# Performance work log

Hardware: AMD Instinct MI355X
Metric: run time of the kernel (lower is better)

The kernel has to match this reference:

```python
import jax, jax.numpy as jnp
import numpy as np

B, L, D = 2, 2048, 1024
H = 16
DH = D // H
DFF = 4096
THETA = 10000.0
EPS = 1e-5


def setup_inputs() -> dict:
    key = jax.random.key(0)
    ks = jax.random.split(key, 6)
    s_qkv = (2.0 / (D + 3 * D)) ** 0.5
    s_o = (2.0 / (D + D)) ** 0.5
    s_ff = (2.0 / (D + DFF)) ** 0.5
    return {
        'x': jax.random.normal(ks[0], (B, L, D), jnp.float32),
        'w_qkv': jax.random.normal(ks[1], (3 * D, D), jnp.float32) * s_qkv,
        'w_o': jax.random.normal(ks[2], (D, D), jnp.float32) * s_o,
        'w1': jax.random.normal(ks[3], (DFF, D), jnp.float32) * s_ff,
        'w2': jax.random.normal(ks[4], (D, DFF), jnp.float32) * s_ff,
        'w3': jax.random.normal(ks[5], (DFF, D), jnp.float32) * s_ff,
        'g1': jnp.ones((D,), jnp.float32),
        'g2': jnp.ones((D,), jnp.float32),
    }


def _rmsnorm(x, g):
    xf = x.astype(jnp.float32)
    inv = jax.lax.rsqrt(jnp.mean(xf * xf, axis=-1, keepdims=True) + EPS)
    return (xf * inv * g).astype(x.dtype)


def _rotate_pair(t):
    # interleaved pairs: (x0,x1,x2,x3,...) -> (-x1,x0,-x3,x2,...)
    t2 = t.reshape(t.shape[:-1] + (t.shape[-1] // 2, 2))
    r = jnp.stack((-t2[..., 1], t2[..., 0]), axis=-1)
    return r.reshape(t.shape)


def reference(x, w_qkv, w_o, w1, w2, w3, g1, g2):
    Bb, Ll, Dd = x.shape
    # --- attention sublayer ---
    y = _rmsnorm(x, g1)
    qkv = y @ w_qkv.T                       # (B, L, 3D)
    q, k, v = jnp.split(qkv, 3, axis=-1)
    def to_heads(t):
        return t.reshape(Bb, Ll, H, DH).transpose(0, 2, 1, 3)  # (B,H,L,Dh)
    q, k, v = to_heads(q), to_heads(k), to_heads(v)
    # RoPE (interleaved), positions = 0..L-1
    inv_freq = 1.0 / (THETA ** (jnp.arange(0, DH, 2, dtype=jnp.float32) / DH))
    ang = jnp.arange(Ll, dtype=jnp.float32)[:, None] * inv_freq  # (L, Dh/2)
    ang = jnp.repeat(ang, 2, axis=-1)                            # (L, Dh)
    cos, sin = jnp.cos(ang), jnp.sin(ang)
    q = q * cos + _rotate_pair(q) * sin
    k = k * cos + _rotate_pair(k) * sin
    att = jnp.einsum('bhqd,bhkd->bhqk', q, k) * (1.0 / np.sqrt(DH))
    causal = jnp.tril(jnp.ones((Ll, Ll), dtype=bool))
    att = jnp.where(causal, att, -jnp.inf)
    att = jax.nn.softmax(att, axis=-1)
    yh = jnp.einsum('bhqk,bhkd->bhqd', att, v)
    y = yh.transpose(0, 2, 1, 3).reshape(Bb, Ll, Dd)
    x = x + y @ w_o.T
    # --- SwiGLU FFN sublayer ---
    y = _rmsnorm(x, g2)
    h = jax.nn.silu(y @ w1.T) * (y @ w3.T)
    return x + h @ w2.T
```

## Files before the change

kernel.cpp:

```cpp
#include <hip/hip_runtime.h>


typedef __attribute__((ext_vector_type(8))) short short8;
typedef __attribute__((ext_vector_type(4))) float f32x4;

#define DEV __device__ __forceinline__

DEV unsigned short f2b(float f) {
  unsigned int u = __builtin_bit_cast(unsigned int, f);
  unsigned int r = u + 0x7fffu + ((u >> 16) & 1u);
  return (unsigned short)(r >> 16);
}
DEV f32x4 MFMA(short8 a, short8 b, f32x4 c) {
  return __builtin_amdgcn_mfma_f32_16x16x32_bf16(a, b, c, 0, 0, 0);
}
DEV void gload16(const void* g, void* lds) {
  __builtin_amdgcn_global_load_lds((const __attribute__((address_space(1))) void*)g,
                                   (__attribute__((address_space(3))) void*)lds, 16, 0, 0);
}

__global__ __launch_bounds__(256) void cvt_k(const float* __restrict__ src,
                                             unsigned short* __restrict__ dst, int n) {
  int i = (blockIdx.x * 256 + threadIdx.x) * 4;
  if (i + 3 < n) {
    float4 v = *(const float4*)(src + i);
    ushort4 o;
    o.x = f2b(v.x); o.y = f2b(v.y); o.z = f2b(v.z); o.w = f2b(v.w);
    *(ushort4*)(dst + i) = o;
  } else {
    for (int c = 0; c < 4 && i + c < n; ++c) dst[i + c] = f2b(src[i + c]);
  }
}

__global__ __launch_bounds__(256) void rope_k(float2* __restrict__ tab) {
  const int i = blockIdx.x * 256 + threadIdx.x;
  const int lt = i >> 5, pr = i & 31;
  const float invf = __expf((float)pr * -0.28782313662425572f);
  const float ang = (float)lt * invf;
  float sn, cs;
  sincosf(ang, &sn, &cs);
  tab[i] = make_float2(cs, sn);
}

__global__ __launch_bounds__(256) void rms_k(const float* __restrict__ x,
                                             const float* __restrict__ g,
                                             unsigned short* __restrict__ out) {
  const int row = blockIdx.x;
  const int t = threadIdx.x;
  const float4 v = *(const float4*)(x + (size_t)row * 1024 + t * 4);
  float ss = v.x * v.x + v.y * v.y + v.z * v.z + v.w * v.w;
#pragma unroll
  for (int m = 32; m >= 1; m >>= 1) ss += __shfl_xor(ss, m, 64);
  __shared__ float red[4];
  if ((t & 63) == 0) red[t >> 6] = ss;
  __syncthreads();
  float tot = red[0] + red[1] + red[2] + red[3];
  float inv = rsqrtf(tot * (1.0f / 1024.0f) + 1e-5f);
  ushort4 o;
  o.x = f2b(v.x * inv * g[t * 4 + 0]);
  o.y = f2b(v.y * inv * g[t * 4 + 1]);
  o.z = f2b(v.z * inv * g[t * 4 + 2]);
  o.w = f2b(v.w * inv * g[t * 4 + 3]);
  *(ushort4*)(out + (size_t)row * 1024 + t * 4) = o;
}

template <int MODE>
__global__ __launch_bounds__(256, 3) void gemm_bt(
    const unsigned short* __restrict__ A, const unsigned short* __restrict__ B0,
    int M, int N, int K,
    float* __restrict__ outF, const float* __restrict__ resid,
    unsigned short* __restrict__ q, unsigned short* __restrict__ k2,
    unsigned short* __restrict__ v,
    const float2* __restrict__ rtab) {
  __shared__ __align__(16) unsigned short As[128 * 32];
  __shared__ __align__(16) unsigned short Bs[128 * 32];
  const int t = threadIdx.x;
  const int wv = t >> 6, ln = t & 63;
  const int l15 = ln & 15, grp = ln >> 4;
  const int wr = wv >> 1, wc = wv & 1;
  const int m0 = blockIdx.y * 128;
  const int n0 = blockIdx.x * 128;

  f32x4 acc[4][4];
#pragma unroll
  for (int mm = 0; mm < 4; ++mm)
#pragma unroll
    for (int nn = 0; nn < 4; ++nn) acc[mm][nn] = (f32x4){0.f, 0.f, 0.f, 0.f};

  for (int k0 = 0; k0 < K; k0 += 32) {
#pragma unroll
    for (int i = 0; i < 2; ++i) {
      const size_t rA = (size_t)(m0 + i * 64 + (t >> 2));
      gload16((const char*)A + (rA * K + k0) * 2 + (t & 3) * 16,
              (char*)As + i * 4096 + wv * 1024);
      const size_t rB = (size_t)(n0 + i * 64 + (t >> 2));
      gload16((const char*)B0 + (rB * K + k0) * 2 + (t & 3) * 16,
              (char*)Bs + i * 4096 + wv * 1024);
    }
    __syncthreads();
    short8 af[4], bf0[4];
#pragma unroll
    for (int mm = 0; mm < 4; ++mm)
      af[mm] = *(const short8*)&As[(wr * 64 + mm * 16 + l15) * 32 + grp * 8];
#pragma unroll
    for (int nn = 0; nn < 4; ++nn)
      bf0[nn] = *(const short8*)&Bs[(wc * 64 + nn * 16 + l15) * 32 + grp * 8];
#pragma unroll
    for (int mm = 0; mm < 4; ++mm)
#pragma unroll
      for (int nn = 0; nn < 4; ++nn) acc[mm][nn] = MFMA(af[mm], bf0[nn], acc[mm][nn]);
    __syncthreads();
  }

#pragma unroll
  for (int mm = 0; mm < 4; ++mm)
#pragma unroll
    for (int nn = 0; nn < 4; ++nn)
#pragma unroll
      for (int j = 0; j < 4; ++j) {
        const int r = m0 + wr * 64 + mm * 16 + grp * 4 + j;
        const int c = n0 + wc * 64 + nn * 16 + l15;
        float val = acc[mm][nn][j];
        if constexpr (MODE == 0) {
          const int mat = c >> 10;
          const int rem = c & 1023;
          const int hh = rem >> 6;
          const int dh = rem & 63;
          const int bt = r >> 11;
          const int lt = r & 2047;
          float outv = val;
          if (mat < 2) {
            const float partner = __shfl_xor(val, 1, 64);
            const float2 cs = rtab[lt * 32 + (dh >> 1)];
            outv = (dh & 1) ? (val * cs.x + partner * cs.y) : (val * cs.x - partner * cs.y);
          }
          unsigned short* dst = (mat == 0) ? q : ((mat == 1) ? k2 : v);
          dst[((size_t)(bt * 16 + hh) * 2048 + lt) * 64 + dh] = f2b(outv);
        } else {
          const size_t idx = (size_t)r * N + c;
          outF[idx] = resid[idx] + val;
        }
      }
}

__global__ __launch_bounds__(512, 2) void ffn_k(
    const unsigned short* __restrict__ A, const unsigned short* __restrict__ B0,
    const unsigned short* __restrict__ B1, unsigned short* __restrict__ outH) {
  __shared__ __align__(16) char Asm[2][32768];
  __shared__ __align__(16) char Bsm[2][32768];
  const int t = threadIdx.x;
  const int wid = t >> 6, lane = t & 63;
  const int l15 = lane & 15, grp = lane >> 4;
  const int wr = wid >> 2, wc = wid & 3;
  const int m0 = blockIdx.y * 256;
  const int n0 = blockIdx.x * 256;

  const char* srcA[4];
  const char* srcB[4];
#pragma unroll
  for (int s = 0; s < 4; ++s) {
    const int lb = s * 8192 + t * 16;
    const int r = lb >> 7;
    const int sw = (((lb >> 4) & 7) * 16) ^ ((r & 7) << 4);
    srcA[s] = (const char*)A + (size_t)(m0 + r) * 2048 + sw;
    const int R = n0 + r;
    const unsigned short* bsrc = ((R >> 4) & 1) ? B1 : B0;
    const int br = ((R >> 5) << 4) + (R & 15);
    srcB[s] = (const char*)bsrc + (size_t)br * 2048 + sw;
  }

  f32x4 acc[8][4];
#pragma unroll
  for (int m = 0; m < 8; ++m)
#pragma unroll
    for (int n = 0; n < 4; ++n) acc[m][n] = (f32x4){0.f, 0.f, 0.f, 0.f};

  gload16(srcA[0], Asm[0] + 0 * 8192 + wid * 1024);
  gload16(srcA[1], Asm[0] + 1 * 8192 + wid * 1024);
  gload16(srcB[0], Bsm[0] + 0 * 8192 + wid * 1024);
  gload16(srcB[1], Bsm[0] + 1 * 8192 + wid * 1024);
  gload16(srcA[2], Asm[0] + 2 * 8192 + wid * 1024);
  gload16(srcA[3], Asm[0] + 3 * 8192 + wid * 1024);
  gload16(srcB[2], Bsm[0] + 2 * 8192 + wid * 1024);
  gload16(srcB[3], Bsm[0] + 3 * 8192 + wid * 1024);

  const int rA0 = wr * 64 + l15;
  const int rB0 = wc * 32 + l15;

#pragma unroll 1
  for (int kt = 0; kt < 16; ++kt) {
    const int cb = kt & 1;
    const size_t koff = (size_t)((kt + 1 < 16) ? (kt + 1) : kt) * 128;
    const char* Ab = Asm[cb];
    const char* Bb = Bsm[cb];
    char* An = Asm[cb ^ 1];
    char* Bn = Bsm[cb ^ 1];

    short8 a0[2][4], a1[2][4], b0[2][2], b1[2][2];

    gload16(srcA[0] + koff, An + 0 * 8192 + wid * 1024);
    gload16(srcA[1] + koff, An + 1 * 8192 + wid * 1024);
    asm volatile("s_waitcnt vmcnt(6)" ::: "memory");
    __builtin_amdgcn_s_barrier();
#pragma unroll
    for (int ks = 0; ks < 2; ++ks)
#pragma unroll
      for (int m = 0; m < 4; ++m) {
        const int r = rA0 + m * 16;
        a0[ks][m] = *(const short8*)(Ab + r * 128 + ((ks * 64 + grp * 16) ^ ((r & 7) << 4)));
      }
#pragma unroll
    for (int ks = 0; ks < 2; ++ks)
#pragma unroll
      for (int n = 0; n < 2; ++n) {
        const int r = rB0 + n * 16;
        b0[ks][n] = *(const short8*)(Bb + r * 128 + ((ks * 64 + grp * 16) ^ ((r & 7) << 4)));
      }
    __builtin_amdgcn_sched_barrier(0);
    __builtin_amdgcn_s_setprio(1);
#pragma unroll
    for (int ks = 0; ks < 2; ++ks)
#pragma unroll
      for (int m = 0; m < 4; ++m)
#pragma unroll
        for (int n = 0; n < 2; ++n) acc[m][n] = MFMA(a0[ks][m], b0[ks][n], acc[m][n]);
    __builtin_amdgcn_s_setprio(0);

    gload16(srcB[0] + koff, Bn + 0 * 8192 + wid * 1024);
    gload16(srcB[1] + koff, Bn + 1 * 8192 + wid * 1024);
    asm volatile("s_waitcnt vmcnt(4)" ::: "memory");
    __builtin_amdgcn_s_barrier();
#pragma unroll
    for (int ks = 0; ks < 2; ++ks)
#pragma unroll
      for (int n = 0; n < 2; ++n) {
        const int r = 128 + rB0 + n * 16;
        b1[ks][n] = *(const short8*)(Bb + r * 128 + ((ks * 64 + grp * 16) ^ ((r & 7) << 4)));
      }
    __builtin_amdgcn_sched_barrier(0);
    __builtin_amdgcn_s_setprio(1);
#pragma unroll
    for (int ks = 0; ks < 2; ++ks)
#pragma unroll
      for (int m = 0; m < 4; ++m)
#pragma unroll
        for (int n = 0; n < 2; ++n) acc[m][2 + n] = MFMA(a0[ks][m], b1[ks][n], acc[m][2 + n]);
    __builtin_amdgcn_s_setprio(0);

    gload16(srcA[2] + koff, An + 2 * 8192 + wid * 1024);
    gload16(srcA[3] + koff, An + 3 * 8192 + wid * 1024);
    __builtin_amdgcn_s_barrier();
#pragma unroll
    for (int ks = 0; ks < 2; ++ks)
#pragma unroll
      for (int m = 0; m < 4; ++m) {
        const int r = 128 + rA0 + m * 16;
        a1[ks][m] = *(const short8*)(Ab + r * 128 + ((ks * 64 + grp * 16) ^ ((r & 7) << 4)));
      }
    __builtin_amdgcn_sched_barrier(0);
    __builtin_amdgcn_s_setprio(1);
#pragma unroll
    for (int ks = 0; ks < 2; ++ks)
#pragma unroll
      for (int m = 0; m < 4; ++m)
#pragma unroll
        for (int n = 0; n < 2; ++n) acc[4 + m][2 + n] = MFMA(a1[ks][m], b1[ks][n], acc[4 + m][2 + n]);
    __builtin_amdgcn_s_setprio(0);

    gload16(srcB[2] + koff, Bn + 2 * 8192 + wid * 1024);
    gload16(srcB[3] + koff, Bn + 3 * 8192 + wid * 1024);
    __builtin_amdgcn_s_barrier();
    __builtin_amdgcn_s_setprio(1);
#pragma unroll
    for (int ks = 0; ks < 2; ++ks)
#pragma unroll
      for (int m = 0; m < 4; ++m)
#pragma unroll
        for (int n = 0; n < 2; ++n) acc[4 + m][n] = MFMA(a1[ks][m], b0[ks][n], acc[4 + m][n]);
    __builtin_amdgcn_s_setprio(0);
  }

#pragma unroll
  for (int mh = 0; mh < 2; ++mh)
#pragma unroll
    for (int m = 0; m < 4; ++m)
#pragma unroll
      for (int nh = 0; nh < 2; ++nh)
#pragma unroll
        for (int j = 0; j < 4; ++j) {
          const int row = m0 + mh * 128 + wr * 64 + m * 16 + grp * 4 + j;
          const int ch = (n0 >> 1) + nh * 64 + wc * 16 + l15;
          const float a1v = acc[mh * 4 + m][nh * 2 + 0][j];
          const float a3v = acc[mh * 4 + m][nh * 2 + 1][j];
          const float hval = a1v / (1.0f + __expf(-a1v)) * a3v;
          outH[(size_t)row * 4096 + ch] = f2b(hval);
        }
}

__global__ __launch_bounds__(256) void vtr_k(const unsigned short* __restrict__ v,
                                             unsigned short* __restrict__ vt) {
  __shared__ __align__(16) unsigned short tile[64][72];
  const int bh = blockIdx.y;
  const int lt0 = blockIdx.x * 64;
  const int t = threadIdx.x;
  const int r = t >> 2;
  const int c0 = (t & 3) * 16;
  const unsigned short* src = v + ((size_t)bh * 2048 + lt0 + r) * 64 + c0;
  *(short8*)&tile[r][c0] = *(const short8*)src;
  *(short8*)&tile[r][c0 + 8] = *(const short8*)(src + 8);
  __syncthreads();
  unsigned short outv[16];
#pragma unroll
  for (int i = 0; i < 16; ++i) outv[i] = tile[c0 + i][r];
  unsigned short* dst = vt + ((size_t)bh * 64 + r) * 2048 + lt0 + c0;
  *(short8*)dst = *(short8*)&outv[0];
  *(short8*)(dst + 8) = *(short8*)&outv[8];
}

__global__ __launch_bounds__(256) void attn_k(const unsigned short* __restrict__ qb,
                                              const unsigned short* __restrict__ kb,
                                              const unsigned short* __restrict__ vt,
                                              unsigned short* __restrict__ yh) {
  const int pair = blockIdx.x;
  const int bh = blockIdx.y;
  const int t = threadIdx.x;
  const int w = t >> 6, lane = t & 63;
  const int l15 = lane & 15, grp = lane >> 4;

  __shared__ __align__(16) char Ks[2][8192];
  __shared__ __align__(16) char Vs[2][8192];
  __shared__ __align__(16) char Ps[8192];
  char* Pw = Ps + w * 2048;

  const char* kg = (const char*)kb + (size_t)bh * 262144;
  const char* vg = (const char*)vt + (size_t)bh * 262144;

  const int lb0 = t * 16, lb1 = 4096 + t * 16;
  const int r0 = lb0 >> 7, r1 = lb1 >> 7;
  const int sl0 = (lb0 & 0x70) ^ ((r0 & 7) << 4);
  const int sl1 = (lb1 & 0x70) ^ ((r1 & 7) << 4);
  const char* srcK0 = kg + r0 * 128 + sl0;
  const char* srcK1 = kg + r1 * 128 + sl1;
  const char* srcV0 = vg + (size_t)r0 * 4096 + sl0;
  const char* srcV1 = vg + (size_t)r1 * 4096 + sl1;

  const int bq = bh >> 4, hh = bh & 15;

#pragma unroll 1
  for (int half = 0; half < 2; ++half) {
    const int qblk = half ? pair : (31 - pair);
    const int qw = qblk * 64 + w * 16;

    const unsigned short* qp = qb + ((size_t)bh * 2048 + qw) * 64;
    const short8 qf0 = *(const short8*)(qp + l15 * 64 + grp * 8);
    const short8 qf1 = *(const short8*)(qp + l15 * 64 + 32 + grp * 8);

    f32x4 o[4];
#pragma unroll
    for (int d = 0; d < 4; ++d) o[d] = (f32x4){0.f, 0.f, 0.f, 0.f};
    float mrun[4], lrun[4];
#pragma unroll
    for (int j = 0; j < 4; ++j) { mrun[j] = -3.0e38f; lrun[j] = 0.f; }

    const int nkt = qblk + 1;

    __syncthreads();
    {
      gload16(srcK0, Ks[0] + w * 1024);
      gload16(srcK1, Ks[0] + 4096 + w * 1024);
      gload16(srcV0, Vs[0] + w * 1024);
      gload16(srcV1, Vs[0] + 4096 + w * 1024);
    }

#pragma unroll 1
    for (int kt = 0; kt < nkt; ++kt) {
      const int par = kt & 1;
      const int ktn = (kt + 1 < nkt) ? (kt + 1) : kt;
      gload16(srcK0 + (size_t)ktn * 8192, Ks[par ^ 1] + w * 1024);
      gload16(srcK1 + (size_t)ktn * 8192, Ks[par ^ 1] + 4096 + w * 1024);
      gload16(srcV0 + ktn * 128, Vs[par ^ 1] + w * 1024);
      gload16(srcV1 + ktn * 128, Vs[par ^ 1] + 4096 + w * 1024);
      asm volatile("s_waitcnt vmcnt(4)" ::: "memory");
      __builtin_amdgcn_s_barrier();

      const char* Kc = Ks[par];
      const char* Vc = Vs[par];

      f32x4 s[4];
#pragma unroll
      for (int c = 0; c < 4; ++c) {
        const int r = c * 16 + l15;
        const int xr = (r & 7) << 4;
        const short8 kf0 = *(const short8*)(Kc + r * 128 + ((grp * 16) ^ xr));
        const short8 kf1 = *(const short8*)(Kc + r * 128 + ((64 + grp * 16) ^ xr));
        f32x4 z = (f32x4){0.f, 0.f, 0.f, 0.f};
        __builtin_amdgcn_s_setprio(1);
        z = MFMA(qf0, kf0, z);
        z = MFMA(qf1, kf1, z);
        __builtin_amdgcn_s_setprio(0);
        s[c] = z;
      }

      const bool diag = (kt == qblk);
      float alpha[4], p[4][4];
#pragma unroll
      for (int j = 0; j < 4; ++j) {
        const int qg = qw + grp * 4 + j;
        float a[4];
#pragma unroll
        for (int c = 0; c < 4; ++c) {
          float av = s[c][j] * 0.125f;
          if (diag && (kt * 64 + c * 16 + l15 > qg)) av = -3.0e38f;
          a[c] = av;
        }
        float mx = fmaxf(fmaxf(a[0], a[1]), fmaxf(a[2], a[3]));
        mx = fmaxf(mx, __shfl_xor(mx, 1, 64));
        mx = fmaxf(mx, __shfl_xor(mx, 2, 64));
        mx = fmaxf(mx, __shfl_xor(mx, 4, 64));
        mx = fmaxf(mx, __shfl_xor(mx, 8, 64));
        const float mnew = fmaxf(mrun[j], mx);
        alpha[j] = __expf(mrun[j] - mnew);
        mrun[j] = mnew;
        float rs = 0.f;
#pragma unroll
        for (int c = 0; c < 4; ++c) {
          const float e = __expf(a[c] - mnew);
          p[c][j] = e;
          rs += e;
        }
        rs += __shfl_xor(rs, 1, 64);
        rs += __shfl_xor(rs, 2, 64);
        rs += __shfl_xor(rs, 4, 64);
        rs += __shfl_xor(rs, 8, 64);
        lrun[j] = lrun[j] * alpha[j] + rs;
      }
#pragma unroll
      for (int d = 0; d < 4; ++d)
#pragma unroll
        for (int j = 0; j < 4; ++j) o[d][j] *= alpha[j];

#pragma unroll
      for (int j = 0; j < 4; ++j) {
        const int r = grp * 4 + j;
        const int xr = (r & 7) << 4;
        char* pr = Pw + r * 128;
#pragma unroll
        for (int c = 0; c < 4; ++c)
          *(unsigned short*)(pr + (((c * 16 + l15) * 2) ^ xr)) = f2b(p[c][j]);
      }
      const int xp = (l15 & 7) << 4;
      const short8 pa0 = *(const short8*)(Pw + l15 * 128 + ((grp * 16) ^ xp));
      const short8 pa1 = *(const short8*)(Pw + l15 * 128 + ((64 + grp * 16) ^ xp));
#pragma unroll
      for (int db = 0; db < 4; ++db) {
        const int rv = db * 16 + l15;
        const int xv = (rv & 7) << 4;
        const short8 vf0 = *(const short8*)(Vc + rv * 128 + ((grp * 16) ^ xv));
        const short8 vf1 = *(const short8*)(Vc + rv * 128 + ((64 + grp * 16) ^ xv));
        __builtin_amdgcn_s_setprio(1);
        o[db] = MFMA(pa0, vf0, o[db]);
        o[db] = MFMA(pa1, vf1, o[db]);
        __builtin_amdgcn_s_setprio(0);
      }
      __builtin_amdgcn_s_barrier();
    }

#pragma unroll
    for (int db = 0; db < 4; ++db)
#pragma unroll
      for (int j = 0; j < 4; ++j) {
        const float valo = o[db][j] / lrun[j];
        const size_t rowo = (size_t)bq * 2048 + qw + grp * 4 + j;
        yh[rowo * 1024 + hh * 64 + db * 16 + l15] = f2b(valo);
      }
  }
}

extern "C" void kernel_launch(void* const* d_in, const int* in_sizes, int n_in,
                              void* d_out, int out_size, void* d_ws, size_t ws_size,
                              hipStream_t stream) {
  const float* x = (const float*)d_in[0];
  const float* wqkv = (const float*)d_in[1];
  const float* wo = (const float*)d_in[2];
  const float* w1 = (const float*)d_in[3];
  const float* w2 = (const float*)d_in[4];
  const float* w3 = (const float*)d_in[5];
  const float* g1 = (const float*)d_in[6];
  const float* g2 = (const float*)d_in[7];

  char* ws = (char*)d_ws;
  unsigned short* wqkv_b = (unsigned short*)(ws + 0);
  unsigned short* wo_b = (unsigned short*)(ws + 6291456);
  unsigned short* w1_b = (unsigned short*)(ws + 8388608);
  unsigned short* w3_b = (unsigned short*)(ws + 16777216);
  unsigned short* w2_b = (unsigned short*)(ws + 25165824);
  float* x2 = (float*)(ws + 33554432);
  float2* rtab = (float2*)(ws + 33554432);
  unsigned short* yb = (unsigned short*)(ws + 50331648);
  unsigned short* qb = (unsigned short*)(ws + 58720256);
  unsigned short* kb = (unsigned short*)(ws + 67108864);
  unsigned short* vb = (unsigned short*)(ws + 75497472);
  unsigned short* vt = (unsigned short*)(ws + 83886080);
  unsigned short* yh = vb;
  unsigned short* hb = (unsigned short*)(ws + 58720256);
  if (ws_size < 92274688) return;

  cvt_k<<<3072, 256, 0, stream>>>(wqkv, wqkv_b, 3145728);
  cvt_k<<<1024, 256, 0, stream>>>(wo, wo_b, 1048576);
  cvt_k<<<4096, 256, 0, stream>>>(w1, w1_b, 4194304);
  cvt_k<<<4096, 256, 0, stream>>>(w3, w3_b, 4194304);
  cvt_k<<<4096, 256, 0, stream>>>(w2, w2_b, 4194304);
  rope_k<<<256, 256, 0, stream>>>(rtab);

  rms_k<<<4096, 256, 0, stream>>>(x, g1, yb);
  gemm_bt<0><<<dim3(24, 32), 256, 0, stream>>>(yb, wqkv_b, 4096, 3072, 1024,
                                               nullptr, nullptr, qb, kb, vb, rtab);
  vtr_k<<<dim3(32, 32), 256, 0, stream>>>(vb, vt);
  attn_k<<<dim3(16, 32), 256, 0, stream>>>(qb, kb, vt, yh);
  gemm_bt<1><<<dim3(8, 32), 256, 0, stream>>>(yh, wo_b, 4096, 1024, 1024,
                                              x2, x, nullptr, nullptr, nullptr, nullptr);
  rms_k<<<4096, 256, 0, stream>>>(x2, g2, yb);
  ffn_k<<<dim3(32, 16), 512, 0, stream>>>(yb, w1_b, w3_b, hb);
  gemm_bt<1><<<dim3(8, 32), 256, 0, stream>>>(hb, w2_b, 4096, 1024, 4096,
                                              (float*)d_out, x2, nullptr, nullptr, nullptr, nullptr);
}
```

Baseline: 327.7 us.

## Split-K the down-projection GEMM and double-buffer LDS in gemm_bt

The final K=4096 GEMM is split into four K-chunks (1024 blocks instead of 256), each writing bf16 partials, and a separate reduction kernel adds them to the residual. The goal is to fill the GPU better on this long-K, small-grid GEMM. gemm_bt and the new kernel also double-buffer LDS tiles with a prefetch and a vmcnt wait, and use an XCD-aware block remap. The cost is a 32MB partial buffer that overlays the converted weights, an extra kernel launch, and bf16 rounding of the partial sums.

```diff
diff --git a/kernel.cpp b/kernel.cpp
--- a/kernel.cpp
+++ b/kernel.cpp
@@ -10,6 +10,9 @@
   unsigned int u = __builtin_bit_cast(unsigned int, f);
   unsigned int r = u + 0x7fffu + ((u >> 16) & 1u);
   return (unsigned short)(r >> 16);
+}
+DEV float b2f(unsigned short h) {
+  return __builtin_bit_cast(float, ((unsigned int)h) << 16);
 }
 DEV f32x4 MFMA(short8 a, short8 b, f32x4 c) {
   return __builtin_amdgcn_mfma_f32_16x16x32_bf16(a, b, c, 0, 0, 0);
@@ -72,14 +75,27 @@
     unsigned short* __restrict__ q, unsigned short* __restrict__ k2,
     unsigned short* __restrict__ v,
     const float2* __restrict__ rtab) {
-  __shared__ __align__(16) unsigned short As[128 * 32];
-  __shared__ __align__(16) unsigned short Bs[128 * 32];
+  __shared__ __align__(16) unsigned short As[2][128 * 32];
+  __shared__ __align__(16) unsigned short Bs[2][128 * 32];
   const int t = threadIdx.x;
   const int wv = t >> 6, ln = t & 63;
   const int l15 = ln & 15, grp = ln >> 4;
   const int wr = wv >> 1, wc = wv & 1;
-  const int m0 = blockIdx.y * 128;
-  const int n0 = blockIdx.x * 128;
+  int m0, n0;
+  if constexpr (MODE == 1) {
+    const int d = blockIdx.y * 8 + blockIdx.x;
+    const int xcd = d & 7, j = d >> 3;
+    m0 = (xcd * 4 + (j >> 3)) * 128;
+    n0 = (j & 7) * 128;
+  } else {
+    m0 = blockIdx.y * 128;
+    n0 = blockIdx.x * 128;
+  }
+
+  const char* sA0 = (const char*)A + ((size_t)(m0 + (t >> 2)) * K + (t & 3) * 8) * 2;
+  const char* sA1 = (const char*)A + ((size_t)(m0 + 64 + (t >> 2)) * K + (t & 3) * 8) * 2;
+  const char* sB0 = (const char*)B0 + ((size_t)(n0 + (t >> 2)) * K + (t & 3) * 8) * 2;
+  const char* sB1 = (const char*)B0 + ((size_t)(n0 + 64 + (t >> 2)) * K + (t & 3) * 8) * 2;
 
   f32x4 acc[4][4];
 #pragma unroll
@@ -87,29 +103,36 @@
 #pragma unroll
     for (int nn = 0; nn < 4; ++nn) acc[mm][nn] = (f32x4){0.f, 0.f, 0.f, 0.f};
 
-  for (int k0 = 0; k0 < K; k0 += 32) {
-#pragma unroll
-    for (int i = 0; i < 2; ++i) {
-      const size_t rA = (size_t)(m0 + i * 64 + (t >> 2));
-      gload16((const char*)A + (rA * K + k0) * 2 + (t & 3) * 16,
-              (char*)As + i * 4096 + wv * 1024);
-      const size_t rB = (size_t)(n0 + i * 64 + (t >> 2));
-      gload16((const char*)B0 + (rB * K + k0) * 2 + (t & 3) * 16,
-              (char*)Bs + i * 4096 + wv * 1024);
-    }
-    __syncthreads();
+  const int KT = K >> 5;
+  gload16(sA0, (char*)As[0] + wv * 1024);
+  gload16(sA1, (char*)As[0] + 4096 + wv * 1024);
+  gload16(sB0, (char*)Bs[0] + wv * 1024);
+  gload16(sB1, (char*)Bs[0] + 4096 + wv * 1024);
+
+#pragma unroll 1
+  for (int kt = 0; kt < KT; ++kt) {
+    const int par = kt & 1;
+    const size_t ko = (size_t)((kt + 1 < KT) ? (kt + 1) : kt) * 64;
+    gload16(sA0 + ko, (char*)As[par ^ 1] + wv * 1024);
+    gload16(sA1 + ko, (char*)As[par ^ 1] + 4096 + wv * 1024);
+    gload16(sB0 + ko, (char*)Bs[par ^ 1] + wv * 1024);
+    gload16(sB1 + ko, (char*)Bs[par ^ 1] + 4096 + wv * 1024);
+    asm volatile("s_waitcnt vmcnt(4)" ::: "memory");
+    __builtin_amdgcn_s_barrier();
+    const unsigned short* Ab = As[par];
+    const unsigned short* Bb = Bs[par];
     short8 af[4], bf0[4];
 #pragma unroll
     for (int mm = 0; mm < 4; ++mm)
-      af[mm] = *(const short8*)&As[(wr * 64 + mm * 16 + l15) * 32 + grp * 8];
+      af[mm] = *(const short8*)&Ab[(wr * 64 + mm * 16 + l15) * 32 + grp * 8];
 #pragma unroll
     for (int nn = 0; nn < 4; ++nn)
-      bf0[nn] = *(const short8*)&Bs[(wc * 64 + nn * 16 + l15) * 32 + grp * 8];
+      bf0[nn] = *(const short8*)&Bb[(wc * 64 + nn * 16 + l15) * 32 + grp * 8];
 #pragma unroll
     for (int mm = 0; mm < 4; ++mm)
 #pragma unroll
       for (int nn = 0; nn < 4; ++nn) acc[mm][nn] = MFMA(af[mm], bf0[nn], acc[mm][nn]);
-    __syncthreads();
+    __builtin_amdgcn_s_barrier();
   }
 
 #pragma unroll
@@ -143,6 +166,92 @@
       }
 }
 
+__global__ __launch_bounds__(256, 3) void gemm_sk(
+    const unsigned short* __restrict__ A, const unsigned short* __restrict__ B0,
+    unsigned short* __restrict__ part) {
+  __shared__ __align__(16) unsigned short As[2][128 * 32];
+  __shared__ __align__(16) unsigned short Bs[2][128 * 32];
+  const int t = threadIdx.x;
+  const int wv = t >> 6, ln = t & 63;
+  const int l15 = ln & 15, grp = ln >> 4;
+  const int wr = wv >> 1, wc = wv & 1;
+  const int d = blockIdx.y * 8 + blockIdx.x;
+  const int xcd = d & 7, j = d >> 3;
+  const int m0 = (xcd * 4 + (j >> 3)) * 128;
+  const int n0 = (j & 7) * 128;
+  const size_t kbase = (size_t)blockIdx.z * 1024;
+
+  const char* sA0 = (const char*)A + ((size_t)(m0 + (t >> 2)) * 4096 + kbase + (t & 3) * 8) * 2;
+  const char* sA1 = (const char*)A + ((size_t)(m0 + 64 + (t >> 2)) * 4096 + kbase + (t & 3) * 8) * 2;
+  const char* sB0 = (const char*)B0 + ((size_t)(n0 + (t >> 2)) * 4096 + kbase + (t & 3) * 8) * 2;
+  const char* sB1 = (const char*)B0 + ((size_t)(n0 + 64 + (t >> 2)) * 4096 + kbase + (t & 3) * 8) * 2;
+
+  f32x4 acc[4][4];
+#pragma unroll
+  for (int mm = 0; mm < 4; ++mm)
+#pragma unroll
+    for (int nn = 0; nn < 4; ++nn) acc[mm][nn] = (f32x4){0.f, 0.f, 0.f, 0.f};
+
+  gload16(sA0, (char*)As[0] + wv * 1024);
+  gload16(sA1, (char*)As[0] + 4096 + wv * 1024);
+  gload16(sB0, (char*)Bs[0] + wv * 1024);
+  gload16(sB1, (char*)Bs[0] + 4096 + wv * 1024);
+
+#pragma unroll 1
+  for (int kt = 0; kt < 32; ++kt) {
+    const int par = kt & 1;
+    const size_t ko = (size_t)((kt + 1 < 32) ? (kt + 1) : kt) * 64;
+    gload16(sA0 + ko, (char*)As[par ^ 1] + wv * 1024);
+    gload16(sA1 + ko, (char*)As[par ^ 1] + 4096 + wv * 1024);
+    gload16(sB0 + ko, (char*)Bs[par ^ 1] + wv * 1024);
+    gload16(sB1 + ko, (char*)Bs[par ^ 1] + 4096 + wv * 1024);
+    asm volatile("s_waitcnt vmcnt(4)" ::: "memory");
+    __builtin_amdgcn_s_barrier();
+    const unsigned short* Ab = As[par];
+    const unsigned short* Bb = Bs[par];
+    short8 af[4], bf0[4];
+#pragma unroll
+    for (int mm = 0; mm < 4; ++mm)
+      af[mm] = *(const short8*)&Ab[(wr * 64 + mm * 16 + l15) * 32 + grp * 8];
+#pragma unroll
+    for (int nn = 0; nn < 4; ++nn)
+      bf0[nn] = *(const short8*)&Bb[(wc * 64 + nn * 16 + l15) * 32 + grp * 8];
+#pragma unroll
+    for (int mm = 0; mm < 4; ++mm)
+#pragma unroll
+      for (int nn = 0; nn < 4; ++nn) acc[mm][nn] = MFMA(af[mm], bf0[nn], acc[mm][nn]);
+    __builtin_amdgcn_s_barrier();
+  }
+
+  unsigned short* pz = part + (size_t)blockIdx.z * 4194304;
+#pragma unroll
+  for (int mm = 0; mm < 4; ++mm)
+#pragma unroll
+    for (int nn = 0; nn < 4; ++nn)
+#pragma unroll
+      for (int j = 0; j < 4; ++j) {
+        const int r = m0 + wr * 64 + mm * 16 + grp * 4 + j;
+        const int c = n0 + wc * 64 + nn * 16 + l15;
+        pz[(size_t)r * 1024 + c] = f2b(acc[mm][nn][j]);
+      }
+}
+
+__global__ __launch_bounds__(256) void red_k(const float* __restrict__ x2,
+                                             const unsigned short* __restrict__ part,
+                                             float* __restrict__ out) {
+  const int i = (blockIdx.x * 256 + threadIdx.x) * 4;
+  float4 r = *(const float4*)(x2 + i);
+#pragma unroll
+  for (int z = 0; z < 4; ++z) {
+    const ushort4 p = *(const ushort4*)(part + (size_t)z * 4194304 + i);
+    r.x += b2f(p.x);
+    r.y += b2f(p.y);
+    r.z += b2f(p.z);
+    r.w += b2f(p.w);
+  }
+  *(float4*)(out + i) = r;
+}
+
 __global__ __launch_bounds__(512, 2) void ffn_k(
     const unsigned short* __restrict__ A, const unsigned short* __restrict__ B0,
     const unsigned short* __restrict__ B1, unsigned short* __restrict__ outH) {
@@ -493,16 +602,17 @@
   unsigned short* wo_b = (unsigned short*)(ws + 6291456);
   unsigned short* w1_b = (unsigned short*)(ws + 8388608);
   unsigned short* w3_b = (unsigned short*)(ws + 16777216);
-  unsigned short* w2_b = (unsigned short*)(ws + 25165824);
+  unsigned short* yb = (unsigned short*)(ws + 25165824);
   float* x2 = (float*)(ws + 33554432);
   float2* rtab = (float2*)(ws + 33554432);
-  unsigned short* yb = (unsigned short*)(ws + 50331648);
+  unsigned short* w2_b = (unsigned short*)(ws + 50331648);
   unsigned short* qb = (unsigned short*)(ws + 58720256);
   unsigned short* kb = (unsigned short*)(ws + 67108864);
   unsigned short* vb = (unsigned short*)(ws + 75497472);
   unsigned short* vt = (unsigned short*)(ws + 83886080);
   unsigned short* yh = vb;
   unsigned short* hb = (unsigned short*)(ws + 58720256);
+  unsigned short* part = (unsigned short*)(ws + 0);
   if (ws_size < 92274688) return;
 
   cvt_k<<<3072, 256, 0, stream>>>(wqkv, wqkv_b, 3145728);
@@ -521,6 +631,6 @@
                                               x2, x, nullptr, nullptr, nullptr, nullptr);
   rms_k<<<4096, 256, 0, stream>>>(x2, g2, yb);
   ffn_k<<<dim3(32, 16), 512, 0, stream>>>(yb, w1_b, w3_b, hb);
-  gemm_bt<1><<<dim3(8, 32), 256, 0, stream>>>(hb, w2_b, 4096, 1024, 4096,
-                                              (float*)d_out, x2, nullptr, nullptr, nullptr, nullptr);
-}
+  gemm_sk<<<dim3(8, 32, 4), 256, 0, stream>>>(hb, w2_b, part);
+  red_k<<<4096, 256, 0, stream>>>(x2, part, (float*)d_out);
+}
```

Measured after the change: 303.4 us. 7.4% less time.
